# Kernel optimization log

Hardware: AMD Instinct MI355X
Metric: run time of the kernel (lower is better)

Reference implementation:

```python
import jax, jax.numpy as jnp
import numpy as np
import math

D_MODEL = 2048
NUM_HEADS = 16
QUERY_GROUPS = 4
HEAD_DIM = D_MODEL // NUM_HEADS  # 128
B, T = 2, 2048


def setup_inputs() -> dict:
    key = jax.random.key(0)
    ks = jax.random.split(key, 9)
    s = 0.02
    return {
        "x": jax.random.normal(ks[0], (B, T, D_MODEL), dtype=jnp.float32),
        "Wq": jax.random.normal(ks[1], (D_MODEL, NUM_HEADS * HEAD_DIM), dtype=jnp.float32) * s,
        "bq": jnp.zeros((NUM_HEADS * HEAD_DIM,), dtype=jnp.float32),
        "Wk": jax.random.normal(ks[2], (D_MODEL, QUERY_GROUPS * HEAD_DIM), dtype=jnp.float32) * s,
        "bk": jnp.zeros((QUERY_GROUPS * HEAD_DIM,), dtype=jnp.float32),
        "Wv": jax.random.normal(ks[3], (D_MODEL, QUERY_GROUPS * HEAD_DIM), dtype=jnp.float32) * s,
        "bv": jnp.zeros((QUERY_GROUPS * HEAD_DIM,), dtype=jnp.float32),
        "Wo": jax.random.normal(ks[4], (D_MODEL, D_MODEL), dtype=jnp.float32) * s,
        "bo": jnp.zeros((D_MODEL,), dtype=jnp.float32),
    }


def reference(x, Wq, bq, Wk, bk, Wv, bv, Wo, bo):
    Bb, Tt, Dd = x.shape
    G, H, hd = QUERY_GROUPS, NUM_HEADS, HEAD_DIM
    m = H // G  # heads per group
    # projections
    q = (x @ Wq + bq).reshape(Bb, Tt, G, m, hd)   # [B,T,G,m,hd]
    k = (x @ Wk + bk).reshape(Bb, Tt, G, hd)      # [B,T,G,hd]
    v = (x @ Wv + bv).reshape(Bb, Tt, G, hd)
    # scores with native group broadcast (no explicit K/V expansion)
    scores = jnp.einsum('btgmd,bsgd->bgmts', q, k) / math.sqrt(hd)  # [B,G,m,T,T]
    p = jax.nn.softmax(scores, axis=-1)
    out = jnp.einsum('bgmts,bsgd->btgmd', p, v).reshape(Bb, Tt, Dd)
    # output projection (dropout is identity in eval / p=0)
    return out @ Wo + bo
```

## Files before the change

kernel.cpp:

```cpp
#include <hip/hip_runtime.h>

#define D_MODEL 2048
#define T_SEQ   2048
#define NBATCH  2
#define NH      16
#define NG      4
#define HD      128
#define NQKV    3072

typedef short bf16x8 __attribute__((ext_vector_type(8)));
typedef float f32x4  __attribute__((ext_vector_type(4)));
typedef float f32x16 __attribute__((ext_vector_type(16)));
typedef short s16x4  __attribute__((ext_vector_type(4)));
typedef unsigned u32x2 __attribute__((ext_vector_type(2)));
typedef unsigned u32x4 __attribute__((ext_vector_type(4)));

__device__ __forceinline__ short f2bf(float f) {
  union { float f; unsigned u; } v; v.f = f;
  unsigned r = v.u + 0x7fffu + ((v.u >> 16) & 1u);
  return (short)(r >> 16);
}

__device__ __forceinline__ float bf2f(short s) {
  union { unsigned u; float f; } v; v.u = ((unsigned)(unsigned short)s) << 16;
  return v.f;
}

__device__ __forceinline__ float fast_exp2(float x) {
#if __has_builtin(__builtin_amdgcn_exp2f)
  return __builtin_amdgcn_exp2f(x);
#else
  return __expf(x * 0.6931471805599453f);
#endif
}

__device__ __forceinline__ unsigned cvt_pk_bf16(float a, float b) {
  unsigned r;
  asm("v_cvt_pk_bf16_f32 %0, %1, %2" : "=v"(r) : "v"(a), "v"(b));
  return r;
}

__device__ __forceinline__ void permlane32_swap(unsigned &a, unsigned &b) {
  asm("v_permlane32_swap_b32 %0, %1" : "+v"(a), "+v"(b));
}

__device__ __forceinline__ void gload16(const void* g, void* l) {
  __builtin_amdgcn_global_load_lds(
      (const __attribute__((address_space(1))) void*)g,
      (__attribute__((address_space(3))) void*)l, 16, 0, 0);
}

__global__ __launch_bounds__(256) void convert_x_kernel(
    const float* __restrict__ x, short* __restrict__ o, int n) {
  int i = (blockIdx.x * 256 + threadIdx.x) * 4;
  if (i >= n) return;
  float4 v = *(const float4*)(x + i);
  s16x4 s;
  s[0] = f2bf(v.x); s[1] = f2bf(v.y); s[2] = f2bf(v.z); s[3] = f2bf(v.w);
  *(s16x4*)(o + i) = s;
}

__global__ __launch_bounds__(256) void wtrans_kernel(
    const float* __restrict__ W, short* __restrict__ dst,
    int K, int N, int rowOff, int dstStride) {
  __shared__ float t[32][33];
  int tx = threadIdx.x & 31, ty = threadIdx.x >> 5;
  int kb = blockIdx.x * 32, nb = blockIdx.y * 32;
#pragma unroll
  for (int i = 0; i < 4; ++i)
    t[ty + 8*i][tx] = W[(long)(kb + ty + 8*i) * N + nb + tx];
  __syncthreads();
#pragma unroll
  for (int i = 0; i < 4; ++i)
    dst[(long)(rowOff + nb + ty + 8*i) * dstStride + kb + tx] = f2bf(t[tx][ty + 8*i]);
}

__global__ __launch_bounds__(256) void vtrans_kernel(
    const short* __restrict__ qkv, short* __restrict__ vt) {
  __shared__ short t[32][33];
  int bg = blockIdx.z; int b = bg >> 2, g = bg & 3;
  int sb = blockIdx.x * 32, db = blockIdx.y * 32;
  int tx = threadIdx.x & 31, ty = threadIdx.x >> 5;
  const short* src = qkv + (long)(b * T_SEQ) * NQKV + D_MODEL + NG * HD + g * HD;
#pragma unroll
  for (int i = 0; i < 4; ++i)
    t[ty + 8*i][tx] = src[(long)(sb + ty + 8*i) * NQKV + db + tx];
  __syncthreads();
  short* dst = vt + ((long)bg * HD + db) * T_SEQ + sb;
#pragma unroll
  for (int i = 0; i < 4; ++i)
    dst[(long)(ty + 8*i) * T_SEQ + tx] = t[tx][ty + 8*i];
}

template <int BN, int MODE>
__global__ __launch_bounds__(512, 2) void gemm256_kernel(
    const short* __restrict__ A, const short* __restrict__ BT,
    const float* __restrict__ b0, const float* __restrict__ b1, const float* __restrict__ b2,
    void* __restrict__ Cout, int M, int N, int K) {
  constexpr int BM = 256, BK = 64;
  constexpr int NFR = BN / 64;
  constexpr int ASZ = BM * BK;
  constexpr int BSZ = BN * BK;
  constexpr int ACH = (ASZ * 2 / 16) / 512;
  constexpr int BCH = (BSZ * 2 / 16) / 512;
  __shared__ __align__(16) short smem[(ASZ + BSZ) * 2];

  const int tid = threadIdx.x;
  const int w = tid >> 6, lane = tid & 63;
  const int l15 = lane & 15, quad = lane >> 4;
  const int wr = w & 1, wc = w >> 1;
  const int nb = blockIdx.x, mb = blockIdx.y;
  const short* Ab = A + (long)mb * BM * K;
  const short* Bb = BT + (long)nb * BN * K;

  f32x4 acc[8][NFR];
#pragma unroll
  for (int i = 0; i < 8; ++i)
#pragma unroll
    for (int j = 0; j < NFR; ++j) acc[i][j] = 0.0f;

  int aoff[ACH], boff[BCH];
#pragma unroll
  for (int i = 0; i < ACH; ++i) {
    int chunk = i * 512 + tid;
    int r = chunk >> 3, c = chunk & 7, gc = c ^ (r & 7);
    aoff[i] = r * K + gc * 8;
  }
#pragma unroll
  for (int i = 0; i < BCH; ++i) {
    int chunk = i * 512 + tid;
    int r = chunk >> 3, c = chunk & 7, gc = c ^ (r & 7);
    boff[i] = r * K + gc * 8;
  }

#pragma unroll
  for (int i = 0; i < ACH; ++i) gload16(Ab + aoff[i], smem + (i * 512 + tid) * 8);
#pragma unroll
  for (int i = 0; i < BCH; ++i) gload16(Bb + boff[i], smem + ASZ + (i * 512 + tid) * 8);

  const int NT = K / BK;
  int cur = 0;
  for (int t = 0; t < NT; ++t) {
    asm volatile("s_waitcnt vmcnt(0)" ::: "memory");
    __builtin_amdgcn_s_barrier();
    asm volatile("" ::: "memory");
    if (t + 1 < NT) {
      const int k0n = (t + 1) * BK;
      short* An = smem + (cur ^ 1) * (ASZ + BSZ);
      short* Bn = An + ASZ;
#pragma unroll
      for (int i = 0; i < ACH; ++i) gload16(Ab + k0n + aoff[i], An + (i * 512 + tid) * 8);
#pragma unroll
      for (int i = 0; i < BCH; ++i) gload16(Bb + k0n + boff[i], Bn + (i * 512 + tid) * 8);
    }
    __builtin_amdgcn_sched_barrier(0);
    const short* As = smem + cur * (ASZ + BSZ);
    const short* Bs = As + ASZ;
#pragma unroll
    for (int ks = 0; ks < 2; ++ks) {
      bf16x8 af[8], bfr[NFR];
#pragma unroll
      for (int i = 0; i < 8; ++i) {
        int r = wr * 128 + i * 16 + l15;
        af[i] = *(const bf16x8*)(As + r * 64 + (((ks * 4 + quad) ^ (r & 7)) * 8));
      }
#pragma unroll
      for (int j = 0; j < NFR; ++j) {
        int r = wc * (NFR * 16) + j * 16 + l15;
        bfr[j] = *(const bf16x8*)(Bs + r * 64 + (((ks * 4 + quad) ^ (r & 7)) * 8));
      }
      __builtin_amdgcn_s_setprio(1);
#pragma unroll
      for (int i = 0; i < 8; ++i)
#pragma unroll
        for (int j = 0; j < NFR; ++j)
          acc[i][j] = __builtin_amdgcn_mfma_f32_16x16x32_bf16(af[i], bfr[j], acc[i][j], 0, 0, 0);
      __builtin_amdgcn_s_setprio(0);
    }
    cur ^= 1;
  }

  float biasv[NFR];
#pragma unroll
  for (int j = 0; j < NFR; ++j) {
    int col = nb * BN + wc * (NFR * 16) + j * 16 + l15;
    float bv;
    if (MODE == 0) {
      if (col < 2048)      bv = b0[col];
      else if (col < 2560) bv = b1[col - 2048];
      else                 bv = b2[col - 2560];
    } else bv = b0[col];
    biasv[j] = bv;
  }
  if (MODE == 0) {
    short* C = (short*)Cout;
#pragma unroll
    for (int i = 0; i < 8; ++i)
#pragma unroll
      for (int j = 0; j < NFR; ++j)
#pragma unroll
        for (int r = 0; r < 4; ++r) {
          int row = mb * BM + wr * 128 + i * 16 + quad * 4 + r;
          int col = nb * BN + wc * (NFR * 16) + j * 16 + l15;
          C[(long)row * N + col] = f2bf(acc[i][j][r] + biasv[j]);
        }
  } else {
    float* C = (float*)Cout;
#pragma unroll
    for (int i = 0; i < 8; ++i)
#pragma unroll
      for (int j = 0; j < NFR; ++j)
#pragma unroll
        for (int r = 0; r < 4; ++r) {
          int row = mb * BM + wr * 128 + i * 16 + quad * 4 + r;
          int col = nb * BN + wc * (NFR * 16) + j * 16 + l15;
          C[(long)row * N + col] = acc[i][j][r] + biasv[j];
        }
  }
}

__global__ __launch_bounds__(256, 2) void attn_kernel(
    const short* __restrict__ qkv, const short* __restrict__ vt,
    short* __restrict__ aout) {
  __shared__ __align__(16) short smem[32768];

  const int tid = threadIdx.x;
  const int w = tid >> 6, lane = tid & 63;
  const int l31 = lane & 31, hi = lane >> 5;
  const int qt = blockIdx.x, h = blockIdx.y, b = blockIdx.z;
  const int g = h >> 2;
  const short* qbase = qkv + (long)(b * T_SEQ + qt * 128) * NQKV + h * HD;
  const short* kbase = qkv + (long)(b * T_SEQ) * NQKV + D_MODEL + g * HD;
  const short* vbase = vt + (long)(b * NG + g) * HD * T_SEQ;
  const float QSCALE = 0.08838834764831845f * 1.4426950408889634f;

  int kroff[4], vroff[4], dst[4];
#pragma unroll
  for (int t = 0; t < 4; ++t) {
    int chunk = w * 256 + t * 64 + lane;
    { int r = chunk >> 4, c = chunk & 15, gc = c ^ (r & 15);
      kroff[t] = r * NQKV + gc * 8; }
    { int r = chunk >> 3, c = chunk & 7, gc = c ^ (r & 7);
      vroff[t] = r * T_SEQ + gc * 8; }
    dst[t] = chunk * 8;
  }

  bf16x8 qfrag[8];
  {
    const short* qrow = qbase + (long)(w * 32 + l31) * NQKV + hi * 8;
#pragma unroll
    for (int ks = 0; ks < 8; ++ks) {
      bf16x8 v = *(const bf16x8*)(qrow + ks * 16);
#pragma unroll
      for (int e = 0; e < 8; ++e) v[e] = f2bf(bf2f(v[e]) * QSCALE);
      qfrag[ks] = v;
    }
  }

#pragma unroll
  for (int t = 0; t < 4; ++t) {
    gload16(kbase + kroff[t], smem + dst[t]);
    gload16(vbase + vroff[t], smem + 8192 + dst[t]);
  }

  f32x16 oaccT[4];
#pragma unroll
  for (int i = 0; i < 4; ++i) oaccT[i] = 0.0f;
  float lpart[4] = {0.f, 0.f, 0.f, 0.f};

  __syncthreads();

  int cur = 0;
  bf16x8 kpre[4], vpre[4];
  for (int st = 0; st < T_SEQ / 64; ++st) {
    const bool pf = (st + 1 < T_SEQ / 64);
    short* Ks = smem + cur * 16384;
    short* Vs = Ks + 8192;
    if (pf) {
      const short* kb2 = kbase + (long)(st + 1) * 64 * NQKV;
      const short* vb2 = vbase + (st + 1) * 64;
#pragma unroll
      for (int t = 0; t < 4; ++t) {
        kpre[t] = *(const bf16x8*)(kb2 + kroff[t]);
        vpre[t] = *(const bf16x8*)(vb2 + vroff[t]);
      }
    }

    f32x16 sacc[2][2];
    sacc[0][0] = 0.0f; sacc[0][1] = 0.0f; sacc[1][0] = 0.0f; sacc[1][1] = 0.0f;
    __builtin_amdgcn_s_setprio(1);
#pragma unroll
    for (int ks = 0; ks < 8; ++ks) {
#pragma unroll
      for (int sb = 0; sb < 2; ++sb) {
        int srow = sb * 32 + l31;
        bf16x8 a = *(const bf16x8*)(Ks + srow * 128 + (((ks * 2 + hi) ^ (srow & 15)) * 8));
        sacc[sb][ks & 1] = __builtin_amdgcn_mfma_f32_32x32x16_bf16(a, qfrag[ks], sacc[sb][ks & 1], 0, 0, 0);
      }
    }
    __builtin_amdgcn_s_setprio(0);

    float p0[16], p1[16];
#pragma unroll
    for (int r = 0; r < 16; ++r) p0[r] = fast_exp2(sacc[0][0][r] + sacc[0][1][r]);
#pragma unroll
    for (int r = 0; r < 16; ++r) p1[r] = fast_exp2(sacc[1][0][r] + sacc[1][1][r]);
#pragma unroll
    for (int r = 0; r < 16; ++r) lpart[r & 3] += p0[r] + p1[r];

    __builtin_amdgcn_s_setprio(1);
#pragma unroll
    for (int k2 = 0; k2 < 4; ++k2) {
      const float* pp = (k2 & 2) ? p1 : p0;
      const int bo = (k2 & 1) * 8;
      unsigned Pa = cvt_pk_bf16(pp[bo + 0], pp[bo + 1]);
      unsigned Pb = cvt_pk_bf16(pp[bo + 2], pp[bo + 3]);
      unsigned Pc = cvt_pk_bf16(pp[bo + 4], pp[bo + 5]);
      unsigned Pd = cvt_pk_bf16(pp[bo + 6], pp[bo + 7]);
      permlane32_swap(Pa, Pc);
      permlane32_swap(Pb, Pd);
      u32x4 pu; pu[0] = Pa; pu[1] = Pb; pu[2] = Pc; pu[3] = Pd;
      bf16x8 pfr = __builtin_bit_cast(bf16x8, pu);
#pragma unroll
      for (int db = 0; db < 4; ++db) {
        int drow = db * 32 + l31;
        bf16x8 a = *(const bf16x8*)(Vs + drow * 64 + (((k2 * 2 + hi) ^ (drow & 7)) * 8));
        oaccT[db] = __builtin_amdgcn_mfma_f32_32x32x16_bf16(a, pfr, oaccT[db], 0, 0, 0);
      }
    }
    __builtin_amdgcn_s_setprio(0);

    if (pf) {
      short* Kn = smem + (cur ^ 1) * 16384;
      short* Vn = Kn + 8192;
#pragma unroll
      for (int t = 0; t < 4; ++t) {
        *(bf16x8*)(Kn + dst[t]) = kpre[t];
        *(bf16x8*)(Vn + dst[t]) = vpre[t];
      }
    }
    __syncthreads();
    cur ^= 1;
  }

  float lsum = (lpart[0] + lpart[1]) + (lpart[2] + lpart[3]);
  float lfull = lsum + __shfl_xor(lsum, 32);
  float inv = 1.0f / lfull;

  short* Osm = smem;
  const int qrl = w * 32 + l31;
  const int swzbase = qrl * 128;
#pragma unroll
  for (int db = 0; db < 4; ++db)
#pragma unroll
    for (int gq = 0; gq < 4; ++gq) {
      unsigned w0 = cvt_pk_bf16(oaccT[db][4 * gq + 0] * inv, oaccT[db][4 * gq + 1] * inv);
      unsigned w1 = cvt_pk_bf16(oaccT[db][4 * gq + 2] * inv, oaccT[db][4 * gq + 3] * inv);
      int c = db * 4 + gq;
      u32x2 wp; wp[0] = w0; wp[1] = w1;
      *(u32x2*)(Osm + swzbase + ((c ^ (qrl & 15)) * 8) + 4 * hi) = wp;
    }
  __syncthreads();

  short* obase = aout + (long)(b * T_SEQ + qt * 128) * D_MODEL + h * HD;
  const int row = tid >> 1, ch = tid & 1;
#pragma unroll
  for (int j = 0; j < 8; ++j) {
    int c2 = ch * 8 + j;
    bf16x8 v = *(const bf16x8*)(Osm + row * 128 + ((c2 ^ (row & 15)) * 8));
    *(bf16x8*)(obase + (long)row * D_MODEL + c2 * 8) = v;
  }
}

extern "C" void kernel_launch(void* const* d_in, const int* in_sizes, int n_in,
                              void* d_out, int out_size, void* d_ws, size_t ws_size,
                              hipStream_t stream) {
  const float* x  = (const float*)d_in[0];
  const float* Wq = (const float*)d_in[1];
  const float* bq = (const float*)d_in[2];
  const float* Wk = (const float*)d_in[3];
  const float* bk = (const float*)d_in[4];
  const float* Wv = (const float*)d_in[5];
  const float* bv = (const float*)d_in[6];
  const float* Wo = (const float*)d_in[7];
  const float* bo = (const float*)d_in[8];

  const long NTOK = (long)NBATCH * T_SEQ;
  short* xb    = (short*)d_ws;
  short* wqkvT = xb + NTOK * D_MODEL;
  short* woT   = wqkvT + (long)NQKV * D_MODEL;
  short* qkvb  = woT + (long)D_MODEL * D_MODEL;
  short* vtb   = qkvb + NTOK * NQKV;
  short* attnb = vtb + (long)NBATCH * NG * HD * T_SEQ;

  int nX = (int)(NTOK * D_MODEL);
  convert_x_kernel<<<nX / (256 * 4), 256, 0, stream>>>(x, xb, nX);
  wtrans_kernel<<<dim3(D_MODEL / 32, D_MODEL / 32), 256, 0, stream>>>(Wq, wqkvT, D_MODEL, D_MODEL, 0, D_MODEL);
  wtrans_kernel<<<dim3(D_MODEL / 32, 512 / 32), 256, 0, stream>>>(Wk, wqkvT, D_MODEL, 512, 2048, D_MODEL);
  wtrans_kernel<<<dim3(D_MODEL / 32, 512 / 32), 256, 0, stream>>>(Wv, wqkvT, D_MODEL, 512, 2560, D_MODEL);
  wtrans_kernel<<<dim3(D_MODEL / 32, D_MODEL / 32), 256, 0, stream>>>(Wo, woT, D_MODEL, D_MODEL, 0, D_MODEL);

  gemm256_kernel<256, 0><<<dim3(NQKV / 256, NTOK / 256), 512, 0, stream>>>(
      xb, wqkvT, bq, bk, bv, (void*)qkvb, (int)NTOK, NQKV, D_MODEL);

  vtrans_kernel<<<dim3(T_SEQ / 32, HD / 32, NBATCH * NG), 256, 0, stream>>>(qkvb, vtb);

  attn_kernel<<<dim3(T_SEQ / 128, NH, NBATCH), 256, 0, stream>>>(qkvb, vtb, attnb);

  gemm256_kernel<128, 1><<<dim3(D_MODEL / 128, NTOK / 256), 512, 0, stream>>>(
      attnb, woT, bo, bo, bo, (void*)d_out, (int)NTOK, D_MODEL, D_MODEL);
}
```

Baseline: 297.1 us.

## Add XCD-aware block swizzle and triple-buffered GEMM for output projection

Adds an XCD swizzle that remaps block ids so consecutive tiles land on the same chiplet, improving L2 reuse in both GEMMs. The output projection GEMM moves to a new kernel with a three-stage LDS ring buffer, prefetching two K-tiles ahead with explicit vmcnt waits and a single barrier per iteration. It also raises MFMA priority during compute. The deeper buffer uses more LDS and is limited to one block per CU, which reduces occupancy in exchange for better latency hiding.

Result: slower. 303.5 us (+2.2%).

```diff
diff --git a/kernel.cpp b/kernel.cpp
--- a/kernel.cpp
+++ b/kernel.cpp
@@ -48,6 +48,16 @@
   __builtin_amdgcn_global_load_lds(
       (const __attribute__((address_space(1))) void*)g,
       (__attribute__((address_space(3))) void*)l, 16, 0, 0);
+}
+
+__device__ __forceinline__ void xcd_swizzle(int &nb, int &mb) {
+  const int gx = gridDim.x;
+  const int nwg = gx * gridDim.y;
+  const int id = blockIdx.y * gx + blockIdx.x;
+  const int cpx = nwg >> 3;
+  const int swz = (id & 7) * cpx + (id >> 3);
+  nb = swz % gx;
+  mb = swz / gx;
 }
 
 __global__ __launch_bounds__(256) void convert_x_kernel(
@@ -109,7 +119,8 @@
   const int w = tid >> 6, lane = tid & 63;
   const int l15 = lane & 15, quad = lane >> 4;
   const int wr = w & 1, wc = w >> 1;
-  const int nb = blockIdx.x, mb = blockIdx.y;
+  int nb, mb;
+  xcd_swizzle(nb, mb);
   const short* Ab = A + (long)mb * BM * K;
   const short* Bb = BT + (long)nb * BN * K;
 
@@ -214,6 +225,141 @@
         for (int r = 0; r < 4; ++r) {
           int row = mb * BM + wr * 128 + i * 16 + quad * 4 + r;
           int col = nb * BN + wc * (NFR * 16) + j * 16 + l15;
+          C[(long)row * N + col] = acc[i][j][r] + biasv[j];
+        }
+  }
+}
+
+template <int MODE>
+__global__ __launch_bounds__(512, 1) void gemm_deep_kernel(
+    const short* __restrict__ A, const short* __restrict__ BT,
+    const float* __restrict__ b0, const float* __restrict__ b1, const float* __restrict__ b2,
+    void* __restrict__ Cout, int M, int N, int K) {
+  constexpr int BM = 256, BN = 128, BK = 64;
+  constexpr int NFR = 2;
+  constexpr int ASZ = BM * BK;
+  constexpr int BSZ = BN * BK;
+  constexpr int BUF = ASZ + BSZ;
+  constexpr int ACH = 4, BCH = 2;
+  __shared__ __align__(16) short smem[BUF * 3];
+
+  const int tid = threadIdx.x;
+  const int w = tid >> 6, lane = tid & 63;
+  const int l15 = lane & 15, quad = lane >> 4;
+  const int wr = w & 1, wc = w >> 1;
+  int nb, mb;
+  xcd_swizzle(nb, mb);
+  const short* Ab = A + (long)mb * BM * K;
+  const short* Bb = BT + (long)nb * BN * K;
+
+  f32x4 acc[8][NFR];
+#pragma unroll
+  for (int i = 0; i < 8; ++i)
+#pragma unroll
+    for (int j = 0; j < NFR; ++j) acc[i][j] = 0.0f;
+
+  int aoff[ACH], boff[BCH];
+#pragma unroll
+  for (int i = 0; i < ACH; ++i) {
+    int chunk = i * 512 + tid;
+    int r = chunk >> 3, c = chunk & 7, gc = c ^ (r & 7);
+    aoff[i] = r * K + gc * 8;
+  }
+#pragma unroll
+  for (int i = 0; i < BCH; ++i) {
+    int chunk = i * 512 + tid;
+    int r = chunk >> 3, c = chunk & 7, gc = c ^ (r & 7);
+    boff[i] = r * K + gc * 8;
+  }
+
+  auto issue = [&](int t, int bi) {
+    const int k0 = t * BK;
+    short* Ad = smem + bi * BUF;
+    short* Bd = Ad + ASZ;
+#pragma unroll
+    for (int i = 0; i < ACH; ++i) gload16(Ab + k0 + aoff[i], Ad + (i * 512 + tid) * 8);
+#pragma unroll
+    for (int i = 0; i < BCH; ++i) gload16(Bb + k0 + boff[i], Bd + (i * 512 + tid) * 8);
+  };
+
+  const int NT = K / BK;
+  issue(0, 0);
+  issue(1, 1);
+
+  int cur = 0;
+  for (int t = 0; t < NT; ++t) {
+    if (t + 1 < NT) {
+      asm volatile("s_waitcnt vmcnt(6)" ::: "memory");
+    } else {
+      asm volatile("s_waitcnt vmcnt(0)" ::: "memory");
+    }
+    __builtin_amdgcn_s_barrier();
+    asm volatile("" ::: "memory");
+    if (t + 2 < NT) {
+      int b2 = cur + 2; if (b2 >= 3) b2 -= 3;
+      issue(t + 2, b2);
+    }
+    __builtin_amdgcn_sched_barrier(0);
+    const short* As = smem + cur * BUF;
+    const short* Bs = As + ASZ;
+#pragma unroll
+    for (int ks = 0; ks < 2; ++ks) {
+      bf16x8 af[8], bfr[NFR];
+#pragma unroll
+      for (int i = 0; i < 8; ++i) {
+        int r = wr * 128 + i * 16 + l15;
+        af[i] = *(const bf16x8*)(As + r * 64 + (((ks * 4 + quad) ^ (r & 7)) * 8));
+      }
+#pragma unroll
+      for (int j = 0; j < NFR; ++j) {
+        int r = wc * 32 + j * 16 + l15;
+        bfr[j] = *(const bf16x8*)(Bs + r * 64 + (((ks * 4 + quad) ^ (r & 7)) * 8));
+      }
+      __builtin_amdgcn_s_setprio(1);
+#pragma unroll
+      for (int i = 0; i < 8; ++i)
+#pragma unroll
+        for (int j = 0; j < NFR; ++j)
+          acc[i][j] = __builtin_amdgcn_mfma_f32_16x16x32_bf16(af[i], bfr[j], acc[i][j], 0, 0, 0);
+      __builtin_amdgcn_s_setprio(0);
+    }
+    ++cur; if (cur >= 3) cur = 0;
+  }
+
+  float biasv[NFR];
+#pragma unroll
+  for (int j = 0; j < NFR; ++j) {
+    int col = nb * BN + wc * 32 + j * 16 + l15;
+    float bv;
+    if (MODE == 0) {
+      if (col < 2048)      bv = b0[col];
+      else if (col < 2560) bv = b1[col - 2048];
+      else                 bv = b2[col - 2560];
+    } else bv = b0[col];
+    biasv[j] = bv;
+  }
+  if (MODE == 0) {
+    short* C = (short*)Cout;
+#pragma unroll
+    for (int i = 0; i < 8; ++i)
+#pragma unroll
+      for (int j = 0; j < NFR; ++j)
+#pragma unroll
+        for (int r = 0; r < 4; ++r) {
+          int row = mb * BM + wr * 128 + i * 16 + quad * 4 + r;
+          int col = nb * BN + wc * 32 + j * 16 + l15;
+          C[(long)row * N + col] = f2bf(acc[i][j][r] + biasv[j]);
+        }
+  } else {
+    float* C = (float*)Cout;
+#pragma unroll
+    for (int i = 0; i < 8; ++i)
+#pragma unroll
+      for (int j = 0; j < NFR; ++j)
+#pragma unroll
+        for (int r = 0; r < 4; ++r) {
+          int row = mb * BM + wr * 128 + i * 16 + quad * 4 + r;
+          int col = nb * BN + wc * 32 + j * 16 + l15;
           C[(long)row * N + col] = acc[i][j][r] + biasv[j];
         }
   }
@@ -407,6 +553,6 @@
 
   attn_kernel<<<dim3(T_SEQ / 128, NH, NBATCH), 256, 0, stream>>>(qkvb, vtb, attnb);
 
-  gemm256_kernel<128, 1><<<dim3(D_MODEL / 128, NTOK / 256), 512, 0, stream>>>(
+  gemm_deep_kernel<1><<<dim3(D_MODEL / 128, NTOK / 256), 512, 0, stream>>>(
       attnb, woT, bo, bo, bo, (void*)d_out, (int)NTOK, D_MODEL, D_MODEL);
 }
```
